# Optimization experiments

Measured on AMD Instinct MI355X. Metric: run time of the kernel, lower is better.

## Reference

```python
import jax, jax.numpy as jnp
import numpy as np

EPS = 1e-6


def setup_inputs() -> dict:
    key = jax.random.key(0)
    k1, k2, k3 = jax.random.split(key, 3)
    B, N1, N2, D, K, C = 8, 1024, 1024, 1, 5, 3
    xa = jax.random.normal(k1, (B, N1, D, C), dtype=jnp.float32)
    features = jax.random.normal(k2, (B, N1, K, C), dtype=jnp.float32)
    xt = jax.random.normal(k3, (B, N2, D, C), dtype=jnp.float32)
    # learned parameter: log_std of shape (in_dims, num_basis, num_channels)
    log_std = jnp.log(1e-6 + 0.1 * jnp.ones((D, K, C), dtype=jnp.float32))
    return {"xa": xa, "features": features, "xt": xt, "log_std": log_std}


def reference(xa, features, xt, log_std):
    # xa: (B, N1, D, C), xt: (B, N2, D, C), features: (B, N1, K, C), log_std: (D, K, C)
    std = jnp.exp(log_std) + EPS                       # (D, K, C)
    x1 = xa[:, :, :, None, :] / std                    # (B, N1, D, K, C)
    x2 = xt[:, :, :, None, :] / std                    # (B, N2, D, K, C)
    sq1 = jnp.sum(x1 * x1, axis=2)                     # (B, N1, K, C)
    sq2 = jnp.sum(x2 * x2, axis=2)                     # (B, N2, K, C)
    # pairwise squared distance per basis/channel
    prod = jnp.einsum('bndkc,bmdkc->bnmkc', x1, x2)    # (B, N1, N2, K, C)
    dist = sq1[:, :, None] + sq2[:, None] - 2.0 * prod # (B, N1, N2, K, C)
    wt = jnp.exp(-0.5 * dist)                          # RBF weights
    # weighted sum over context points N1
    smoothed = jnp.einsum('bnkc,bnmkc->bmkc', features, wt)  # (B, N2, K, C)
    return smoothed
```

## Files before the change

kernel.cpp:

```cpp
#include <hip/hip_runtime.h>

#define EPS_F 1e-6f
#define LOG2E 1.4426950408889634f

typedef float f4a __attribute__((ext_vector_type(4), aligned(16)));

__device__ __forceinline__ float rfl(float x) {
    return __builtin_bit_cast(float, __builtin_amdgcn_readfirstlane(__builtin_bit_cast(int, x)));
}

__global__ __launch_bounds__(256, 4) void icgp_partial_kernel(
    const float* __restrict__ xa,
    const float* __restrict__ feat,
    const float* __restrict__ xt,
    const float* __restrict__ log_std,
    float* __restrict__ pws)
{
    __shared__ float lds[3840];

    const int bid  = blockIdx.x;
    const int mt   = bid & 15;
    const int nc   = (bid >> 4) & 15;
    const int b    = bid >> 8;
    const int tid  = threadIdx.x;
    const int wv   = __builtin_amdgcn_readfirstlane(tid >> 6);
    const int lane = tid & 63;
    const int m    = mt * 64 + lane;
    const int n0   = nc * 64;

    const float* __restrict__ fg = feat + ((size_t)b * 1024 + n0) * 15;
    if (tid < 240) {
        const f4a v = *(const f4a*)(fg + tid * 4);
        #pragma unroll
        for (int e = 0; e < 4; ++e) {
            const int g = tid * 4 + e;
            const int r = g / 15, c = g - r * 15;
            lds[r * 16 + c] = v[e];
        }
    }
    const float* __restrict__ ag = xa + ((size_t)b * 1024 + n0) * 3;
    if (tid < 48) {
        const f4a v = *(const f4a*)(ag + tid * 4);
        #pragma unroll
        for (int e = 0; e < 4; ++e) {
            const int g = tid * 4 + e;
            const int r = g / 3, c = g - r * 3;
            lds[1024 + r * 4 + c] = v[e];
        }
    }

    float coef[15];
    #pragma unroll
    for (int kc = 0; kc < 15; ++kc) {
        const float s = __expf(log_std[kc]) + EPS_F;
        coef[kc] = rfl(-0.5f * LOG2E / (s * s));
    }
    bool uni = true;
    #pragma unroll
    for (int k = 1; k < 5; ++k)
        #pragma unroll
        for (int c = 0; c < 3; ++c)
            uni = uni && (coef[k * 3 + c] == coef[c]);

    const float t0 = xt[(b * 1024 + m) * 3 + 0];
    const float t1 = xt[(b * 1024 + m) * 3 + 1];
    const float t2 = xt[(b * 1024 + m) * 3 + 2];

    __syncthreads();

    float acc[15];
    #pragma unroll
    for (int kc = 0; kc < 15; ++kc) acc[kc] = 0.0f;

    const int rb = wv * 16;

    if (uni) {
        const float c0 = coef[0], c1 = coef[1], c2 = coef[2];
        #pragma unroll 4
        for (int i = 0; i < 16; ++i) {
            const float* __restrict__ row = &lds[(rb + i) * 16];
            const f4a fA = *(const f4a*)(row);
            const f4a fB = *(const f4a*)(row + 4);
            const f4a fC = *(const f4a*)(row + 8);
            const f4a fD = *(const f4a*)(row + 12);
            const f4a av = *(const f4a*)(&lds[1024 + (rb + i) * 4]);
            float d0 = av.x - t0; d0 *= d0;
            float d1 = av.y - t1; d1 *= d1;
            float d2 = av.z - t2; d2 *= d2;
            const float w0 = __builtin_amdgcn_exp2f(d0 * c0);
            const float w1 = __builtin_amdgcn_exp2f(d1 * c1);
            const float w2 = __builtin_amdgcn_exp2f(d2 * c2);
            acc[0]  += w0 * fA.x;  acc[1]  += w1 * fA.y;  acc[2]  += w2 * fA.z;
            acc[3]  += w0 * fA.w;  acc[4]  += w1 * fB.x;  acc[5]  += w2 * fB.y;
            acc[6]  += w0 * fB.z;  acc[7]  += w1 * fB.w;  acc[8]  += w2 * fC.x;
            acc[9]  += w0 * fC.y;  acc[10] += w1 * fC.z;  acc[11] += w2 * fC.w;
            acc[12] += w0 * fD.x;  acc[13] += w1 * fD.y;  acc[14] += w2 * fD.z;
        }
    } else {
        for (int i = 0; i < 16; ++i) {
            const float* __restrict__ row = &lds[(rb + i) * 16];
            float fv[16];
            *(f4a*)(fv)      = *(const f4a*)(row);
            *(f4a*)(fv + 4)  = *(const f4a*)(row + 4);
            *(f4a*)(fv + 8)  = *(const f4a*)(row + 8);
            *(f4a*)(fv + 12) = *(const f4a*)(row + 12);
            const f4a av = *(const f4a*)(&lds[1024 + (rb + i) * 4]);
            float dd[3];
            dd[0] = av.x - t0; dd[0] *= dd[0];
            dd[1] = av.y - t1; dd[1] *= dd[1];
            dd[2] = av.z - t2; dd[2] *= dd[2];
            #pragma unroll
            for (int k = 0; k < 5; ++k)
                #pragma unroll
                for (int c = 0; c < 3; ++c)
                    acc[k * 3 + c] +=
                        __builtin_amdgcn_exp2f(dd[c] * coef[k * 3 + c]) * fv[k * 3 + c];
        }
    }

    __syncthreads();
    #pragma unroll
    for (int kc = 0; kc < 15; ++kc) lds[tid * 15 + kc] = acc[kc];
    __syncthreads();

    float* __restrict__ pb = pws + (size_t)nc * 122880
                                 + ((size_t)b * 1024 + mt * 64) * 15;
    #pragma unroll
    for (int j = 0; j < 4; ++j) {
        const int oidx = j * 256 + tid;
        if (oidx < 960) {
            const int mm = oidx / 15, kc = oidx - mm * 15;
            float s = 0.0f;
            #pragma unroll
            for (int w = 0; w < 4; ++w)
                s += lds[(w * 64 + mm) * 15 + kc];
            pb[oidx] = s;
        }
    }
}

__global__ __launch_bounds__(256) void icgp_reduce_kernel(
    const float* __restrict__ pws, float* __restrict__ out)
{
    const int idx4 = blockIdx.x * 256 + threadIdx.x;
    const f4a* __restrict__ p4 = (const f4a*)pws;
    f4a s = {0.0f, 0.0f, 0.0f, 0.0f};
    #pragma unroll
    for (int ns = 0; ns < 16; ++ns) {
        const f4a v = p4[(size_t)ns * 30720 + idx4];
        s.x += v.x; s.y += v.y; s.z += v.z; s.w += v.w;
    }
    ((f4a*)out)[idx4] = s;
}

extern "C" void kernel_launch(void* const* d_in, const int* in_sizes, int n_in,
                              void* d_out, int out_size, void* d_ws, size_t ws_size,
                              hipStream_t stream) {
    const float* xa      = (const float*)d_in[0];
    const float* feat    = (const float*)d_in[1];
    const float* xt      = (const float*)d_in[2];
    const float* log_std = (const float*)d_in[3];
    float* out = (float*)d_out;
    float* pws = (float*)d_ws;

    icgp_partial_kernel<<<dim3(2048), dim3(256), 0, stream>>>(xa, feat, xt, log_std, pws);
    icgp_reduce_kernel<<<dim3(120), dim3(256), 0, stream>>>(pws, out);
}
```

Baseline: 77.15 us.

## Register-block four target points per thread to reuse LDS feature loads

Each thread now handles four target points instead of one, so every feature row and xa value read from LDS is reused across four accumulator sets. The grid shrinks from 2048 to 512 blocks, LDS grows to hold per-wave partials for 256 targets, and launch bounds drop to 2 blocks per SIMD group to allow the extra registers. This trades occupancy and block count for less LDS traffic per exp/FMA. With only 512 blocks on a 256-CU part, the work may be spread unevenly across the machine.

```diff
diff --git a/kernel.cpp b/kernel.cpp
--- a/kernel.cpp
+++ b/kernel.cpp
@@ -9,23 +9,23 @@
     return __builtin_bit_cast(float, __builtin_amdgcn_readfirstlane(__builtin_bit_cast(int, x)));
 }
 
-__global__ __launch_bounds__(256, 4) void icgp_partial_kernel(
+__global__ __launch_bounds__(256, 2) void icgp_partial_kernel(
     const float* __restrict__ xa,
     const float* __restrict__ feat,
     const float* __restrict__ xt,
     const float* __restrict__ log_std,
     float* __restrict__ pws)
 {
-    __shared__ float lds[3840];
+    __shared__ float lds[16640];
+    const int SF = 15360, SA = 16384;
 
     const int bid  = blockIdx.x;
-    const int mt   = bid & 15;
-    const int nc   = (bid >> 4) & 15;
-    const int b    = bid >> 8;
+    const int nc   = bid & 15;
+    const int mg   = (bid >> 4) & 3;
+    const int b    = bid >> 6;
     const int tid  = threadIdx.x;
     const int wv   = __builtin_amdgcn_readfirstlane(tid >> 6);
     const int lane = tid & 63;
-    const int m    = mt * 64 + lane;
     const int n0   = nc * 64;
 
     const float* __restrict__ fg = feat + ((size_t)b * 1024 + n0) * 15;
@@ -35,7 +35,7 @@
         for (int e = 0; e < 4; ++e) {
             const int g = tid * 4 + e;
             const int r = g / 15, c = g - r * 15;
-            lds[r * 16 + c] = v[e];
+            lds[SF + r * 16 + c] = v[e];
         }
     }
     const float* __restrict__ ag = xa + ((size_t)b * 1024 + n0) * 3;
@@ -45,7 +45,7 @@
         for (int e = 0; e < 4; ++e) {
             const int g = tid * 4 + e;
             const int r = g / 3, c = g - r * 3;
-            lds[1024 + r * 4 + c] = v[e];
+            lds[SA + r * 4 + c] = v[e];
         }
     }
 
@@ -62,80 +62,93 @@
         for (int c = 0; c < 3; ++c)
             uni = uni && (coef[k * 3 + c] == coef[c]);
 
-    const float t0 = xt[(b * 1024 + m) * 3 + 0];
-    const float t1 = xt[(b * 1024 + m) * 3 + 1];
-    const float t2 = xt[(b * 1024 + m) * 3 + 2];
+    float t[4][3];
+    #pragma unroll
+    for (int p = 0; p < 4; ++p) {
+        const int m = mg * 256 + p * 64 + lane;
+        t[p][0] = xt[(b * 1024 + m) * 3 + 0];
+        t[p][1] = xt[(b * 1024 + m) * 3 + 1];
+        t[p][2] = xt[(b * 1024 + m) * 3 + 2];
+    }
 
     __syncthreads();
 
-    float acc[15];
+    float acc[4][15];
     #pragma unroll
-    for (int kc = 0; kc < 15; ++kc) acc[kc] = 0.0f;
+    for (int p = 0; p < 4; ++p)
+        #pragma unroll
+        for (int kc = 0; kc < 15; ++kc) acc[p][kc] = 0.0f;
 
     const int rb = wv * 16;
 
     if (uni) {
         const float c0 = coef[0], c1 = coef[1], c2 = coef[2];
-        #pragma unroll 4
+        #pragma unroll 2
         for (int i = 0; i < 16; ++i) {
-            const float* __restrict__ row = &lds[(rb + i) * 16];
+            const float* __restrict__ row = &lds[SF + (rb + i) * 16];
             const f4a fA = *(const f4a*)(row);
             const f4a fB = *(const f4a*)(row + 4);
             const f4a fC = *(const f4a*)(row + 8);
             const f4a fD = *(const f4a*)(row + 12);
-            const f4a av = *(const f4a*)(&lds[1024 + (rb + i) * 4]);
-            float d0 = av.x - t0; d0 *= d0;
-            float d1 = av.y - t1; d1 *= d1;
-            float d2 = av.z - t2; d2 *= d2;
-            const float w0 = __builtin_amdgcn_exp2f(d0 * c0);
-            const float w1 = __builtin_amdgcn_exp2f(d1 * c1);
-            const float w2 = __builtin_amdgcn_exp2f(d2 * c2);
-            acc[0]  += w0 * fA.x;  acc[1]  += w1 * fA.y;  acc[2]  += w2 * fA.z;
-            acc[3]  += w0 * fA.w;  acc[4]  += w1 * fB.x;  acc[5]  += w2 * fB.y;
-            acc[6]  += w0 * fB.z;  acc[7]  += w1 * fB.w;  acc[8]  += w2 * fC.x;
-            acc[9]  += w0 * fC.y;  acc[10] += w1 * fC.z;  acc[11] += w2 * fC.w;
-            acc[12] += w0 * fD.x;  acc[13] += w1 * fD.y;  acc[14] += w2 * fD.z;
+            const f4a av = *(const f4a*)(&lds[SA + (rb + i) * 4]);
+            #pragma unroll
+            for (int p = 0; p < 4; ++p) {
+                float d0 = av.x - t[p][0]; d0 *= d0;
+                float d1 = av.y - t[p][1]; d1 *= d1;
+                float d2 = av.z - t[p][2]; d2 *= d2;
+                const float w0 = __builtin_amdgcn_exp2f(d0 * c0);
+                const float w1 = __builtin_amdgcn_exp2f(d1 * c1);
+                const float w2 = __builtin_amdgcn_exp2f(d2 * c2);
+                acc[p][0]  += w0 * fA.x;  acc[p][1]  += w1 * fA.y;  acc[p][2]  += w2 * fA.z;
+                acc[p][3]  += w0 * fA.w;  acc[p][4]  += w1 * fB.x;  acc[p][5]  += w2 * fB.y;
+                acc[p][6]  += w0 * fB.z;  acc[p][7]  += w1 * fB.w;  acc[p][8]  += w2 * fC.x;
+                acc[p][9]  += w0 * fC.y;  acc[p][10] += w1 * fC.z;  acc[p][11] += w2 * fC.w;
+                acc[p][12] += w0 * fD.x;  acc[p][13] += w1 * fD.y;  acc[p][14] += w2 * fD.z;
+            }
         }
     } else {
         for (int i = 0; i < 16; ++i) {
-            const float* __restrict__ row = &lds[(rb + i) * 16];
+            const float* __restrict__ row = &lds[SF + (rb + i) * 16];
             float fv[16];
             *(f4a*)(fv)      = *(const f4a*)(row);
             *(f4a*)(fv + 4)  = *(const f4a*)(row + 4);
             *(f4a*)(fv + 8)  = *(const f4a*)(row + 8);
             *(f4a*)(fv + 12) = *(const f4a*)(row + 12);
-            const f4a av = *(const f4a*)(&lds[1024 + (rb + i) * 4]);
-            float dd[3];
-            dd[0] = av.x - t0; dd[0] *= dd[0];
-            dd[1] = av.y - t1; dd[1] *= dd[1];
-            dd[2] = av.z - t2; dd[2] *= dd[2];
+            const f4a av = *(const f4a*)(&lds[SA + (rb + i) * 4]);
             #pragma unroll
-            for (int k = 0; k < 5; ++k)
+            for (int p = 0; p < 4; ++p) {
+                float dd[3];
+                dd[0] = av.x - t[p][0]; dd[0] *= dd[0];
+                dd[1] = av.y - t[p][1]; dd[1] *= dd[1];
+                dd[2] = av.z - t[p][2]; dd[2] *= dd[2];
                 #pragma unroll
-                for (int c = 0; c < 3; ++c)
-                    acc[k * 3 + c] +=
-                        __builtin_amdgcn_exp2f(dd[c] * coef[k * 3 + c]) * fv[k * 3 + c];
+                for (int k = 0; k < 5; ++k)
+                    #pragma unroll
+                    for (int c = 0; c < 3; ++c)
+                        acc[p][k * 3 + c] +=
+                            __builtin_amdgcn_exp2f(dd[c] * coef[k * 3 + c]) * fv[k * 3 + c];
+            }
         }
     }
 
     __syncthreads();
     #pragma unroll
-    for (int kc = 0; kc < 15; ++kc) lds[tid * 15 + kc] = acc[kc];
+    for (int p = 0; p < 4; ++p)
+        #pragma unroll
+        for (int kc = 0; kc < 15; ++kc)
+            lds[wv * 3840 + (p * 64 + lane) * 15 + kc] = acc[p][kc];
     __syncthreads();
 
     float* __restrict__ pb = pws + (size_t)nc * 122880
-                                 + ((size_t)b * 1024 + mt * 64) * 15;
+                                 + ((size_t)b * 1024 + mg * 256) * 15;
     #pragma unroll
-    for (int j = 0; j < 4; ++j) {
+    for (int j = 0; j < 15; ++j) {
         const int oidx = j * 256 + tid;
-        if (oidx < 960) {
-            const int mm = oidx / 15, kc = oidx - mm * 15;
-            float s = 0.0f;
-            #pragma unroll
-            for (int w = 0; w < 4; ++w)
-                s += lds[(w * 64 + mm) * 15 + kc];
-            pb[oidx] = s;
-        }
+        float s = 0.0f;
+        #pragma unroll
+        for (int w = 0; w < 4; ++w)
+            s += lds[w * 3840 + oidx];
+        pb[oidx] = s;
     }
 }
 
@@ -163,6 +176,6 @@
     float* out = (float*)d_out;
     float* pws = (float*)d_ws;
 
-    icgp_partial_kernel<<<dim3(2048), dim3(256), 0, stream>>>(xa, feat, xt, log_std, pws);
+    icgp_partial_kernel<<<dim3(512), dim3(256), 0, stream>>>(xa, feat, xt, log_std, pws);
     icgp_reduce_kernel<<<dim3(120), dim3(256), 0, stream>>>(pws, out);
 }
```

Result: faster. 74.16 us (-3.9%).
